# Optimization experiments

Hardware: AMD Instinct MI355X
Metric: run time of the kernel (lower is better)

The kernel has to match this reference:

```python
import jax, jax.numpy as jnp
import numpy as np

N_NODES = 10000
T = 8
F_IN = 4
H1 = 16
HEADS = 4
H2 = 32
G = 32
PW = 16
E = 160000


def _gat(x, src, dst, W, a_src, a_dst, b, concat):
    # x: [T, N, Fin]; PyG GATConv (eval mode, dropout inactive), self-loops already in src/dst
    t, n, _ = x.shape
    heads, c = a_src.shape
    z = (x @ W).reshape(t, n, heads, c)                      # [T,N,H,C]
    asrc = jnp.einsum('tnhc,hc->tnh', z, a_src)
    adst = jnp.einsum('tnhc,hc->tnh', z, a_dst)
    e = jax.nn.leaky_relu(asrc[:, src] + adst[:, dst], 0.2)   # [T,E,H]
    e = e.transpose(1, 0, 2)                                  # [E,T,H]
    m = jax.ops.segment_max(e, dst, num_segments=n)           # [N,T,H]
    ex = jnp.exp(e - m[dst])
    s = jax.ops.segment_sum(ex, dst, num_segments=n)
    att = ex / s[dst]                                         # [E,T,H] softmax over in-edges of dst
    msg = z.transpose(1, 0, 2, 3)[src] * att[..., None]       # [E,T,H,C]
    out = jax.ops.segment_sum(msg, dst, num_segments=n)       # [N,T,H,C]
    out = out.transpose(1, 0, 2, 3)                           # [T,N,H,C]
    out = out.reshape(t, n, heads * c) if concat else out.mean(axis=2)
    return out + b


def _forward(dynamic, cI, cR, N, I, R, edge_index, h0,
             W1, att_src1, att_dst1, b1, W2, att_src2, att_dst2, b2,
             W_ih, W_hh, b_ih, b_hh, Wi, bi, Wr, br, Ws, bs):
    Npop = N.squeeze()
    loops = jnp.arange(N_NODES, dtype=edge_index.dtype)
    src = jnp.concatenate([edge_index[0], loops])
    dst = jnp.concatenate([edge_index[1], loops])
    x = dynamic.transpose(1, 0, 2)                            # [T,N,F] all timesteps batched
    x = jax.nn.elu(_gat(x, src, dst, W1, att_src1, att_dst1, b1, True))
    x = jax.nn.elu(_gat(x, src, dst, W2, att_src2, att_dst2, b2, False))
    cur_h = x.mean(axis=1)                                    # [T,H2]

    def gru_step(h, xt):  # torch GRUCell: gates in (r,z,n) order
        gi = W_ih @ xt + b_ih
        gh = W_hh @ h + b_hh
        ir, iz, inn = jnp.split(gi, 3)
        hr, hz, hn = jnp.split(gh, 3)
        r = jax.nn.sigmoid(ir + hr)
        zg = jax.nn.sigmoid(iz + hz)
        ng = jnp.tanh(inn + r * hn)
        hnew = (1.0 - zg) * ng + zg * h
        return hnew, hnew

    h_final, hs = jax.lax.scan(gru_step, h0[0], cur_h)        # hs: [T,G]
    hc = jnp.concatenate([hs, cI[:, None], cR[:, None]], axis=1)  # [T,G+2]
    new_I = (hc @ Wi.T + bi)[None]                            # [1,T,PW]
    new_R = (hc @ Wr.T + br)[None]
    sir = hc @ Ws.T + bs                                      # [T,2]
    alpha = jax.nn.sigmoid(sir[:, 0])
    beta = jax.nn.sigmoid(sir[:, 1])

    def sir_step(carry, _):
        lI, lR = carry
        lS = Npop - lI - lR
        dI = alpha * lI * (lS / Npop) - beta * lI
        dR = beta * lI
        # original accumulates detached increments
        return (lI + jax.lax.stop_gradient(dI), lR + jax.lax.stop_gradient(dR)), (dI, dR)

    _, (dIs, dRs) = jax.lax.scan(sir_step, (I, R), None, length=PW)  # [PW,T]
    phy_I = dIs.T[None]                                       # [1,T,PW]
    phy_R = dRs.T[None]
    return new_I, new_R, phy_I, phy_R, h_final[None]


def setup_inputs() -> dict:
    key = jax.random.key(0)
    ks = jax.random.split(key, 20)
    rn = lambda k, s, sc=0.1: (jax.random.normal(k, s) * sc).astype(jnp.float32)
    return {
        'dynamic': jax.random.normal(ks[0], (N_NODES, T, F_IN), jnp.float32),
        'cI': jax.random.uniform(ks[1], (T,), jnp.float32),
        'cR': jax.random.uniform(ks[2], (T,), jnp.float32),
        'N': jnp.ones((1,), jnp.float32) * 1e6,
        'I': jax.random.uniform(ks[3], (T,), jnp.float32) * 1e4,
        'R': jax.random.uniform(ks[4], (T,), jnp.float32) * 1e4,
        'edge_index': jax.random.randint(ks[5], (2, E), 0, N_NODES, dtype=jnp.int32),
        'h0': rn(ks[6], (1, G)),
        'W1': rn(ks[7], (F_IN, HEADS * H1)),
        'att_src1': rn(ks[8], (HEADS, H1)),
        'att_dst1': rn(ks[9], (HEADS, H1)),
        'b1': jnp.zeros((HEADS * H1,), jnp.float32),
        'W2': rn(ks[10], (HEADS * H1, H2)),
        'att_src2': rn(ks[11], (1, H2)),
        'att_dst2': rn(ks[12], (1, H2)),
        'b2': jnp.zeros((H2,), jnp.float32),
        'W_ih': rn(ks[13], (3 * G, H2)),
        'W_hh': rn(ks[14], (3 * G, G)),
        'b_ih': jnp.zeros((3 * G,), jnp.float32),
        'b_hh': jnp.zeros((3 * G,), jnp.float32),
        'Wi': rn(ks[15], (PW, G + 2)),
        'bi': jnp.zeros((PW,), jnp.float32),
        'Wr': rn(ks[16], (PW, G + 2)),
        'br': jnp.zeros((PW,), jnp.float32),
        'Ws': rn(ks[17], (2, G + 2)),
        'bs': jnp.zeros((2,), jnp.float32),
    }


def reference(dynamic, cI, cR, N, I, R, edge_index, h0,
              W1, att_src1, att_dst1, b1, W2, att_src2, att_dst2, b2,
              W_ih, W_hh, b_ih, b_hh, Wi, bi, Wr, br, Ws, bs):
    return _forward(dynamic, cI, cR, N, I, R, edge_index, h0,
                    W1, att_src1, att_dst1, b1, W2, att_src2, att_dst2, b2,
                    W_ih, W_hh, b_ih, b_hh, Wi, bi, Wr, br, Ws, bs)
```

## Files before the change

kernel.cpp:

```cpp
#include <hip/hip_runtime.h>

#define N_NODES 10000
#define T_STEPS 8
#define F_IN 4
#define H1 16
#define HEADS 4
#define H2 32
#define G 32
#define PW 16
#define E_EDGES 160000
#define CAP 64
#define NREP 32

__device__ __forceinline__ float lrelu(float x) { return x > 0.f ? x : 0.2f * x; }
__device__ __forceinline__ float eluf(float x) { return x > 0.f ? x : (expf(x) - 1.f); }
__device__ __forceinline__ float sigmoidf(float x) { return 1.f / (1.f + expf(-x)); }
__device__ __forceinline__ float g8sum(float v) {
    v += __shfl_xor(v, 8);
    v += __shfl_xor(v, 16);
    v += __shfl_xor(v, 32);
    return v;
}
__device__ __forceinline__ float bf2f(unsigned int u) {
    return __uint_as_float(u << 16);
}
__device__ __forceinline__ unsigned short f2bf(float f) {
    unsigned b = __float_as_uint(f);
    return (unsigned short)((b + 0x7FFFu + ((b >> 16) & 1u)) >> 16);
}

__global__ void __launch_bounds__(256) k_scatter(
        const int* __restrict__ ei, int* __restrict__ cnt, int* __restrict__ colsrc,
        float* __restrict__ part, const unsigned* __restrict__ poison) {
    const unsigned P = *poison;
    int idx = blockIdx.x * 256 + threadIdx.x;
    if (idx < NREP * 256) part[idx] = 0.f;
    if (idx >= E_EDGES) return;
    int src = ei[idx];
    int dst = ei[E_EDGES + idx];
    unsigned pos = (unsigned)atomicAdd(&cnt[dst], 1) - P;
    if (pos < CAP) colsrc[(dst << 6) + pos] = src;
}

__global__ void __launch_bounds__(256) k_l1_node(
        const int* __restrict__ cnt, const int* __restrict__ colsrc,
        const float4* __restrict__ dyn, const float* __restrict__ W1,
        const float* __restrict__ as1, const float* __restrict__ ad1,
        const float* __restrict__ b1, const float* __restrict__ W2,
        const float* __restrict__ as2, const float* __restrict__ ad2,
        unsigned short* __restrict__ z2g, float* __restrict__ asrc2,
        float* __restrict__ adst2, const unsigned* __restrict__ poison) {
    __shared__ float sVA[16], sVD[16];
    __shared__ float sW1[256], sB1[64], sW2[64 * 32];
    __shared__ float sAs2[32], sAd2[32];
    __shared__ float sRow[4][8 * 72];
    const unsigned P = *poison;
    int tid = threadIdx.x;
    int lane = tid & 63, wslot = tid >> 6;
    int n = blockIdx.x * 4 + wslot;
    int t = lane & 7, es = lane >> 3;
    int beg = n << 6;
    unsigned dreal = (unsigned)cnt[n] - P; if (dreal > 63) dreal = 63;
    int deg = (int)dreal + 1;
    const float4 xo = dyn[(n << 3) + t];
    int srcs[8];
#pragma unroll
    for (int k = 0; k < 8; ++k) {
        int e = k * 8 + es;
        srcs[k] = (e < deg - 1) ? colsrc[beg + e] : n;
    }
    {
        const float4* W2v = (const float4*)W2;
        float4* sW2v = (float4*)sW2;
#pragma unroll
        for (int i = tid; i < 512; i += 256) sW2v[i] = W2v[i];
    }
    sW1[tid] = W1[tid];
    if (tid < 64) sB1[tid] = b1[tid];
    if (tid < 32) { sAs2[tid] = as2[tid]; sAd2[tid] = ad2[tid]; }
    if (tid < 32) {
        int q = tid & 15, d = q >> 2, hh = q & 3;
        const float* a = (tid < 16) ? as1 : ad1;
        float acc = 0.f;
#pragma unroll
        for (int c = 0; c < 16; ++c) acc += W1[d * 64 + hh * 16 + c] * a[hh * 16 + c];
        if (tid < 16) sVA[q] = acc;
        else sVD[q] = acc;
    }
    __syncthreads();

    float ad0 = xo.x * sVD[0] + xo.y * sVD[4] + xo.z * sVD[8]  + xo.w * sVD[12];
    float ad1v = xo.x * sVD[1] + xo.y * sVD[5] + xo.z * sVD[9]  + xo.w * sVD[13];
    float ad2v = xo.x * sVD[2] + xo.y * sVD[6] + xo.z * sVD[10] + xo.w * sVD[14];
    float ad3v = xo.x * sVD[3] + xo.y * sVD[7] + xo.z * sVD[11] + xo.w * sVD[15];

    float s0 = 0.f, s1 = 0.f, s2 = 0.f, s3 = 0.f;
    float u[16];
#pragma unroll
    for (int i = 0; i < 16; ++i) u[i] = 0.f;

    int kIters = (deg + 7) >> 3;
    for (int k = 0; k < kIters; ++k) {
        int e = k * 8 + es;
        bool act = e < deg;
        int src = srcs[k];
        const float4 x4 = dyn[(src << 3) + t];
        float l0 = x4.x * sVA[0] + x4.y * sVA[4] + x4.z * sVA[8]  + x4.w * sVA[12] + ad0;
        float l1 = x4.x * sVA[1] + x4.y * sVA[5] + x4.z * sVA[9]  + x4.w * sVA[13] + ad1v;
        float l2 = x4.x * sVA[2] + x4.y * sVA[6] + x4.z * sVA[10] + x4.w * sVA[14] + ad2v;
        float l3 = x4.x * sVA[3] + x4.y * sVA[7] + x4.z * sVA[11] + x4.w * sVA[15] + ad3v;
        float w0 = act ? __expf(lrelu(l0)) : 0.f;
        float w1 = act ? __expf(lrelu(l1)) : 0.f;
        float w2 = act ? __expf(lrelu(l2)) : 0.f;
        float w3 = act ? __expf(lrelu(l3)) : 0.f;
        s0 += w0; s1 += w1; s2 += w2; s3 += w3;
        u[0]  += w0 * x4.x; u[1]  += w0 * x4.y; u[2]  += w0 * x4.z; u[3]  += w0 * x4.w;
        u[4]  += w1 * x4.x; u[5]  += w1 * x4.y; u[6]  += w1 * x4.z; u[7]  += w1 * x4.w;
        u[8]  += w2 * x4.x; u[9]  += w2 * x4.y; u[10] += w2 * x4.z; u[11] += w2 * x4.w;
        u[12] += w3 * x4.x; u[13] += w3 * x4.y; u[14] += w3 * x4.z; u[15] += w3 * x4.w;
    }
    float red[20];
#pragma unroll
    for (int h2 = 0; h2 < 4; ++h2) {
        red[h2 * 5 + 0] = u[h2 * 4 + 0];
        red[h2 * 5 + 1] = u[h2 * 4 + 1];
        red[h2 * 5 + 2] = u[h2 * 4 + 2];
        red[h2 * 5 + 3] = u[h2 * 4 + 3];
    }
    red[4] = s0; red[9] = s1; red[14] = s2; red[19] = s3;
    bool lowHalf = (es < 4);
    float keep[10];
#pragma unroll
    for (int k = 0; k < 10; ++k) {
        float send = lowHalf ? red[10 + k] : red[k];
        float mine = lowHalf ? red[k] : red[10 + k];
        keep[k] = mine + __shfl_xor(send, 32);
    }
    bool firstPair = ((es & 2) == 0);
    float keep2[5];
#pragma unroll
    for (int k = 0; k < 5; ++k) {
        float send = firstPair ? keep[5 + k] : keep[k];
        float mine = firstPair ? keep[k] : keep[5 + k];
        keep2[k] = mine + __shfl_xor(send, 16);
    }
#pragma unroll
    for (int k = 0; k < 5; ++k) keep2[k] += __shfl_xor(keep2[k], 8);
    float uh0 = keep2[0], uh1 = keep2[1], uh2 = keep2[2], uh3 = keep2[3];
    float inv = 1.f / keep2[4];

    float4 ra, rb;
#pragma unroll
    for (int j = 0; j < 8; ++j) {
        int c = es * 8 + j;
        float acc = uh0 * sW1[c] + uh1 * sW1[64 + c] + uh2 * sW1[128 + c] + uh3 * sW1[192 + c];
        float v = eluf(acc * inv + sB1[c]);
        if (j < 4) ((float*)&ra)[j] = v;
        else ((float*)&rb)[j - 4] = v;
    }
    *reinterpret_cast<float4*>(&sRow[wslot][t * 72 + es * 8]) = ra;
    *reinterpret_cast<float4*>(&sRow[wslot][t * 72 + es * 8 + 4]) = rb;
    asm volatile("s_waitcnt lgkmcnt(0)" ::: "memory");
    float z0 = 0.f, z1v = 0.f, z2v = 0.f, z3v = 0.f;
#pragma unroll 8
    for (int j = 0; j < 64; ++j) {
        float r = sRow[wslot][t * 72 + j];
        const float4 w4 = *reinterpret_cast<const float4*>(&sW2[j * 32 + es * 4]);
        z0 += r * w4.x; z1v += r * w4.y; z2v += r * w4.z; z3v += r * w4.w;
    }
    int wid8 = (n << 3) + t;
    unsigned int p0 = (unsigned)f2bf(z0) | ((unsigned)f2bf(z1v) << 16);
    unsigned int p1 = (unsigned)f2bf(z2v) | ((unsigned)f2bf(z3v) << 16);
    *reinterpret_cast<uint2*>(z2g + (size_t)wid8 * 32 + es * 4) = make_uint2(p0, p1);
    float pa = z0 * sAs2[es * 4] + z1v * sAs2[es * 4 + 1] + z2v * sAs2[es * 4 + 2] + z3v * sAs2[es * 4 + 3];
    float pd = z0 * sAd2[es * 4] + z1v * sAd2[es * 4 + 1] + z2v * sAd2[es * 4 + 2] + z3v * sAd2[es * 4 + 3];
    pa = g8sum(pa);
    pd = g8sum(pd);
    if (es == 0) { asrc2[wid8] = pa; adst2[wid8] = pd; }
}

__global__ void __launch_bounds__(256) k_l2_node(
        const int* __restrict__ cnt, const int* __restrict__ colsrc,
        const float* __restrict__ asrc, const float* __restrict__ adst,
        const unsigned short* __restrict__ z2, const float* __restrict__ b2,
        float* __restrict__ part, const unsigned* __restrict__ poison) {
    __shared__ int sSrc[4][64];
    __shared__ float sW[4][64 * 8];
    __shared__ float sS[4][8];
    __shared__ float sB2[32];
    __shared__ float sPart[256];
    const unsigned P = *poison;
    int tid = threadIdx.x;
    int lane = tid & 63, wslot = tid >> 6;
    int n = blockIdx.x * 4 + wslot;
    int t = lane & 7, es = lane >> 3;
    int t2 = lane >> 3, cg = lane & 7;
    int beg = n << 6;
    unsigned dreal = (unsigned)cnt[n] - P; if (dreal > 63) dreal = 63;
    int deg = (int)dreal + 1;
    float ad = adst[(n << 3) + t];
    int srcs2[8];
#pragma unroll
    for (int r = 0; r < 8; ++r) {
        int e = r * 8 + es;
        srcs2[r] = (e < deg - 1) ? colsrc[beg + e] : n;
    }
    if (tid < 32) sB2[tid] = b2[tid];
    sPart[tid] = 0.f;
    __syncthreads();

    int R = (deg + 7) >> 3;
    float ws = 0.f;
#pragma unroll
    for (int r = 0; r < 8; ++r) {
        if (r < R) {
            int e = r * 8 + es;
            int src = srcs2[r];
            float w = (e < deg) ? __expf(lrelu(asrc[(src << 3) + t] + ad)) : 0.f;
            ws += w;
            sW[wslot][e * 8 + t] = w;
            if (t == 0) sSrc[wslot][e] = src;
        }
    }
    float s = g8sum(ws);
    if (es == 0) sS[wslot][t] = s;
    asm volatile("s_waitcnt lgkmcnt(0)" ::: "memory");

    const unsigned short* zb = z2 + t2 * 32 + cg * 4;
    float a0 = 0.f, a1 = 0.f, a2 = 0.f, a3 = 0.f;
    for (int e = 0; e < deg; ++e) {
        int src = sSrc[wslot][e];
        float w = sW[wslot][e * 8 + t2];
        uint2 pz = *reinterpret_cast<const uint2*>(zb + (size_t)src * 256);
        a0 += w * bf2f(pz.x & 0xFFFFu);
        a1 += w * bf2f(pz.x >> 16);
        a2 += w * bf2f(pz.y & 0xFFFFu);
        a3 += w * bf2f(pz.y >> 16);
    }
    float invs = 1.f / sS[wslot][t2];
    int cbase = cg * 4;
    float v0 = eluf(a0 * invs + sB2[cbase]);
    float v1 = eluf(a1 * invs + sB2[cbase + 1]);
    float v2 = eluf(a2 * invs + sB2[cbase + 2]);
    float v3 = eluf(a3 * invs + sB2[cbase + 3]);
    int pidx = t2 * 32 + cbase;
    atomicAdd(&sPart[pidx], v0);
    atomicAdd(&sPart[pidx + 1], v1);
    atomicAdd(&sPart[pidx + 2], v2);
    atomicAdd(&sPart[pidx + 3], v3);
    __syncthreads();
    atomicAdd(&part[((blockIdx.x & (NREP - 1)) << 8) + tid], sPart[tid]);
}

__global__ void k_head(const float* __restrict__ part, const float* __restrict__ h0,
                       const float* __restrict__ W_ih, const float* __restrict__ W_hh,
                       const float* __restrict__ b_ih, const float* __restrict__ b_hh,
                       const float* __restrict__ Wi, const float* __restrict__ bi,
                       const float* __restrict__ Wr, const float* __restrict__ br,
                       const float* __restrict__ Ws, const float* __restrict__ bs,
                       const float* __restrict__ cI, const float* __restrict__ cR,
                       const float* __restrict__ Nptr, const float* __restrict__ Ivec,
                       const float* __restrict__ Rvec, float* __restrict__ out) {
    __shared__ float xs[256];
    __shared__ float h[32], gi[96], gh[96], hnew[32], hs[T_STEPS * 32], sirv[16];
    const float invN = 1.0f / (float)N_NODES;
    int j = threadIdx.x;
    {
        float sx = 0.f, sy = 0.f;
        const float2* p2 = (const float2*)part;
        for (int r = 0; r < NREP; ++r) {
            float2 v = p2[r * 128 + j];
            sx += v.x; sy += v.y;
        }
        xs[2 * j] = sx * invN;
        xs[2 * j + 1] = sy * invN;
    }
    if (j < 32) h[j] = h0[j];
    __syncthreads();
    for (int t = 0; t < T_STEPS; ++t) {
        if (j < 96) {
            float accI = b_ih[j], accH = b_hh[j];
            for (int k = 0; k < 32; ++k) {
                accI += W_ih[j * 32 + k] * xs[t * 32 + k];
                accH += W_hh[j * 32 + k] * h[k];
            }
            gi[j] = accI;
            gh[j] = accH;
        }
        __syncthreads();
        if (j < 32) {
            float r = sigmoidf(gi[j] + gh[j]);
            float zg = sigmoidf(gi[32 + j] + gh[32 + j]);
            float ng = tanhf(gi[64 + j] + r * gh[64 + j]);
            hnew[j] = (1.f - zg) * ng + zg * h[j];
        }
        __syncthreads();
        if (j < 32) {
            h[j] = hnew[j];
            hs[t * 32 + j] = hnew[j];
        }
        __syncthreads();
    }
    if (j < 32) out[512 + j] = h[j];
    {
        int t = j >> 4, p = j & 15;
        float accI = bi[p], accR = br[p];
        for (int k = 0; k < 34; ++k) {
            float hck = (k < 32) ? hs[t * 32 + k] : (k == 32 ? cI[t] : cR[t]);
            accI += hck * Wi[p * 34 + k];
            accR += hck * Wr[p * 34 + k];
        }
        out[j] = accI;
        out[128 + j] = accR;
    }
    if (j < 16) {
        int t = j >> 1, q = j & 1;
        float acc = bs[q];
        for (int k = 0; k < 34; ++k) {
            float hck = (k < 32) ? hs[t * 32 + k] : (k == 32 ? cI[t] : cR[t]);
            acc += hck * Ws[q * 34 + k];
        }
        sirv[j] = acc;
    }
    __syncthreads();
    if (j < 8) {
        int t = j;
        float alpha = sigmoidf(sirv[2 * t]);
        float beta = sigmoidf(sirv[2 * t + 1]);
        float Np = Nptr[0];
        float lI = Ivec[t], lR = Rvec[t];
        for (int p = 0; p < PW; ++p) {
            float lS = Np - lI - lR;
            float dI = alpha * lI * (lS / Np) - beta * lI;
            float dR = beta * lI;
            out[256 + t * 16 + p] = dI;
            out[384 + t * 16 + p] = dR;
            lI += dI;
            lR += dR;
        }
    }
}

extern "C" void kernel_launch(void* const* d_in, const int* in_sizes, int n_in,
                              void* d_out, int out_size, void* d_ws, size_t ws_size,
                              hipStream_t stream) {
    const float* dyn = (const float*)d_in[0];
    const float* cI = (const float*)d_in[1];
    const float* cR = (const float*)d_in[2];
    const float* Nptr = (const float*)d_in[3];
    const float* Ivec = (const float*)d_in[4];
    const float* Rvec = (const float*)d_in[5];
    const int* ei = (const int*)d_in[6];
    const float* h0 = (const float*)d_in[7];
    const float* W1 = (const float*)d_in[8];
    const float* as1 = (const float*)d_in[9];
    const float* ad1 = (const float*)d_in[10];
    const float* b1 = (const float*)d_in[11];
    const float* W2 = (const float*)d_in[12];
    const float* as2 = (const float*)d_in[13];
    const float* ad2 = (const float*)d_in[14];
    const float* b2 = (const float*)d_in[15];
    const float* W_ih = (const float*)d_in[16];
    const float* W_hh = (const float*)d_in[17];
    const float* b_ih = (const float*)d_in[18];
    const float* b_hh = (const float*)d_in[19];
    const float* Wi = (const float*)d_in[20];
    const float* bi = (const float*)d_in[21];
    const float* Wr = (const float*)d_in[22];
    const float* br = (const float*)d_in[23];
    const float* Ws = (const float*)d_in[24];
    const float* bs = (const float*)d_in[25];
    float* out = (float*)d_out;

    char* ws = (char*)d_ws;
    size_t off = 0;
    auto alloc = [&](size_t bytes) {
        void* p = ws + off;
        off += (bytes + 255) & ~(size_t)255;
        return p;
    };
    const size_t TN = (size_t)T_STEPS * N_NODES;
    int* cnt = (int*)alloc(N_NODES * 4);
    float* part = (float*)alloc((size_t)NREP * 256 * 4);
    unsigned short* z2 = (unsigned short*)alloc(TN * 32 * 2);
    float* asrc2 = (float*)alloc(TN * 4);
    float* adst2 = (float*)alloc(TN * 4);
    int* colsrc = (int*)alloc((size_t)N_NODES * CAP * 4);
    unsigned* poison = (unsigned*)alloc(4);
    (void)ws_size; (void)in_sizes; (void)n_in; (void)out_size;

    const int BT = 256;
    int gEdge = (E_EDGES + BT - 1) / BT;
    k_scatter<<<gEdge, BT, 0, stream>>>(ei, cnt, colsrc, part, poison);
    k_l1_node<<<N_NODES / 4, BT, 0, stream>>>(cnt, colsrc, (const float4*)dyn,
                                              W1, as1, ad1, b1, W2, as2, ad2,
                                              z2, asrc2, adst2, poison);
    k_l2_node<<<N_NODES / 4, BT, 0, stream>>>(cnt, colsrc, asrc2, adst2, z2, b2, part, poison);
    k_head<<<1, 128, 0, stream>>>(part, h0, W_ih, W_hh, b_ih, b_hh, Wi, bi, Wr, br, Ws, bs,
                                  cI, cR, Nptr, Ivec, Rvec, out);
}
```

Before: 176.0 us.

## Split layer-2 edge gather across half-waves with 16-byte loads; vectorize z2 projection

The layer-2 aggregation now has each half-wavefront handle alternate edges, with each lane loading 8 bf16 values (16 bytes) per edge instead of 4. This halves the serial dependent loop length over in-degree, and the two halves' partial sums are combined with a cross-lane shuffle. The layer-1 epilogue's 64-wide dot product is fully unrolled and reads the row with float4 LDS loads. ELU switches to fast __expf. The changes add register pressure and a little extra shuffle work, and __expf slightly reduces accuracy.

Result: no change. 172.9 us, median of 2 (-1.8%).

```diff
diff --git a/kernel.cpp b/kernel.cpp
--- a/kernel.cpp
+++ b/kernel.cpp
@@ -13,7 +13,7 @@
 #define NREP 32
 
 __device__ __forceinline__ float lrelu(float x) { return x > 0.f ? x : 0.2f * x; }
-__device__ __forceinline__ float eluf(float x) { return x > 0.f ? x : (expf(x) - 1.f); }
+__device__ __forceinline__ float eluf(float x) { return x > 0.f ? x : (__expf(x) - 1.f); }
 __device__ __forceinline__ float sigmoidf(float x) { return 1.f / (1.f + expf(-x)); }
 __device__ __forceinline__ float g8sum(float v) {
     v += __shfl_xor(v, 8);
@@ -162,11 +162,17 @@
     *reinterpret_cast<float4*>(&sRow[wslot][t * 72 + es * 8 + 4]) = rb;
     asm volatile("s_waitcnt lgkmcnt(0)" ::: "memory");
     float z0 = 0.f, z1v = 0.f, z2v = 0.f, z3v = 0.f;
-#pragma unroll 8
-    for (int j = 0; j < 64; ++j) {
-        float r = sRow[wslot][t * 72 + j];
-        const float4 w4 = *reinterpret_cast<const float4*>(&sW2[j * 32 + es * 4]);
-        z0 += r * w4.x; z1v += r * w4.y; z2v += r * w4.z; z3v += r * w4.w;
+#pragma unroll
+    for (int j = 0; j < 64; j += 4) {
+        float4 r4 = *reinterpret_cast<const float4*>(&sRow[wslot][t * 72 + j]);
+        const float4 w0 = *reinterpret_cast<const float4*>(&sW2[(j + 0) * 32 + es * 4]);
+        const float4 w1 = *reinterpret_cast<const float4*>(&sW2[(j + 1) * 32 + es * 4]);
+        const float4 w2 = *reinterpret_cast<const float4*>(&sW2[(j + 2) * 32 + es * 4]);
+        const float4 w3 = *reinterpret_cast<const float4*>(&sW2[(j + 3) * 32 + es * 4]);
+        z0  += r4.x * w0.x + r4.y * w1.x + r4.z * w2.x + r4.w * w3.x;
+        z1v += r4.x * w0.y + r4.y * w1.y + r4.z * w2.y + r4.w * w3.y;
+        z2v += r4.x * w0.z + r4.y * w1.z + r4.z * w2.z + r4.w * w3.z;
+        z3v += r4.x * w0.w + r4.y * w1.w + r4.z * w2.w + r4.w * w3.w;
     }
     int wid8 = (n << 3) + t;
     unsigned int p0 = (unsigned)f2bf(z0) | ((unsigned)f2bf(z1v) << 16);
@@ -194,7 +200,6 @@
     int lane = tid & 63, wslot = tid >> 6;
     int n = blockIdx.x * 4 + wslot;
     int t = lane & 7, es = lane >> 3;
-    int t2 = lane >> 3, cg = lane & 7;
     int beg = n << 6;
     unsigned dreal = (unsigned)cnt[n] - P; if (dreal > 63) dreal = 63;
     int deg = (int)dreal + 1;
@@ -226,28 +231,40 @@
     if (es == 0) sS[wslot][t] = s;
     asm volatile("s_waitcnt lgkmcnt(0)" ::: "memory");
 
-    const unsigned short* zb = z2 + t2 * 32 + cg * 4;
-    float a0 = 0.f, a1 = 0.f, a2 = 0.f, a3 = 0.f;
-    for (int e = 0; e < deg; ++e) {
-        int src = sSrc[wslot][e];
-        float w = sW[wslot][e * 8 + t2];
-        uint2 pz = *reinterpret_cast<const uint2*>(zb + (size_t)src * 256);
-        a0 += w * bf2f(pz.x & 0xFFFFu);
-        a1 += w * bf2f(pz.x >> 16);
-        a2 += w * bf2f(pz.y & 0xFFFFu);
-        a3 += w * bf2f(pz.y >> 16);
-    }
+    int eo = lane >> 5;
+    int t2 = (lane >> 2) & 7;
+    int cg4 = lane & 3;
+    const unsigned short* zb = z2 + t2 * 32 + cg4 * 8;
+    float a[8];
+#pragma unroll
+    for (int k = 0; k < 8; ++k) a[k] = 0.f;
+    int iters = (deg + 1) >> 1;
+    for (int i = 0; i < iters; ++i) {
+        int e = 2 * i + eo;
+        bool act = e < deg;
+        int ee = act ? e : 0;
+        int src = sSrc[wslot][ee];
+        float w = act ? sW[wslot][ee * 8 + t2] : 0.f;
+        uint4 pz = *reinterpret_cast<const uint4*>(zb + (size_t)src * 256);
+        a[0] += w * bf2f(pz.x & 0xFFFFu);
+        a[1] += w * bf2f(pz.x >> 16);
+        a[2] += w * bf2f(pz.y & 0xFFFFu);
+        a[3] += w * bf2f(pz.y >> 16);
+        a[4] += w * bf2f(pz.z & 0xFFFFu);
+        a[5] += w * bf2f(pz.z >> 16);
+        a[6] += w * bf2f(pz.w & 0xFFFFu);
+        a[7] += w * bf2f(pz.w >> 16);
+    }
+#pragma unroll
+    for (int k = 0; k < 8; ++k) a[k] += __shfl_xor(a[k], 32);
     float invs = 1.f / sS[wslot][t2];
-    int cbase = cg * 4;
-    float v0 = eluf(a0 * invs + sB2[cbase]);
-    float v1 = eluf(a1 * invs + sB2[cbase + 1]);
-    float v2 = eluf(a2 * invs + sB2[cbase + 2]);
-    float v3 = eluf(a3 * invs + sB2[cbase + 3]);
+    int cbase = cg4 * 8 + eo * 4;
+    int koff = eo * 4;
     int pidx = t2 * 32 + cbase;
-    atomicAdd(&sPart[pidx], v0);
-    atomicAdd(&sPart[pidx + 1], v1);
-    atomicAdd(&sPart[pidx + 2], v2);
-    atomicAdd(&sPart[pidx + 3], v3);
+    atomicAdd(&sPart[pidx],     eluf(a[koff]     * invs + sB2[cbase]));
+    atomicAdd(&sPart[pidx + 1], eluf(a[koff + 1] * invs + sB2[cbase + 1]));
+    atomicAdd(&sPart[pidx + 2], eluf(a[koff + 2] * invs + sB2[cbase + 2]));
+    atomicAdd(&sPart[pidx + 3], eluf(a[koff + 3] * invs + sB2[cbase + 3]));
     __syncthreads();
     atomicAdd(&part[((blockIdx.x & (NREP - 1)) << 8) + tid], sPart[tid]);
 }
```
